# Performance work log

Hardware: AMD Instinct MI355X
Metric: run time of the kernel (lower is better)

Reference implementation:

```python
import jax, jax.numpy as jnp
import numpy as np

MU, SIGMA = -9.1232, 3.5412
FFT_SIZES = [8, 16, 32, 64]
HOP_SIZES = [2, 4, 8, 16]
EPS_MAG, EPS_SC = 1e-7, 1e-8


def hann_periodic(n):
    # torch.hann_window default (periodic=True)
    return 0.5 * (1.0 - jnp.cos(2.0 * jnp.pi * jnp.arange(n, dtype=jnp.float32) / n))


def stft_mag(xf, n_fft, hop):
    # xf: (rows, T). Matches torch.stft(center=True, pad_mode='reflect', onesided).
    pad = n_fft // 2
    xp = jnp.pad(xf, ((0, 0), (pad, pad)), mode='reflect')
    n_frames = 1 + (xp.shape[-1] - n_fft) // hop
    idx = jnp.arange(n_frames)[:, None] * hop + jnp.arange(n_fft)[None, :]
    frames = xp[:, idx] * hann_periodic(n_fft)  # (rows, n_frames, n_fft)
    spec = jnp.fft.rfft(frames, axis=-1)        # (rows, n_frames, n_fft//2+1)
    return jnp.abs(spec) + EPS_MAG


def setup_inputs() -> dict:
    key = jax.random.key(0)
    k1, k2 = jax.random.split(key)
    x = jax.random.normal(k1, (32, 1, 128, 1024), dtype=jnp.float32)
    y = jax.random.normal(k2, (32, 1, 128, 1024), dtype=jnp.float32)
    return {"x": x, "y": y}


def reference(x, y):
    B, C, F_mel, T = x.shape
    x_flat = jnp.exp(x * SIGMA + MU).reshape(-1, T)  # un-normalize log-mel -> linear
    y_flat = jnp.exp(y * SIGMA + MU).reshape(-1, T)
    loss_sc = jnp.float32(0.0)
    loss_mag = jnp.float32(0.0)
    for n_fft, hop in zip(FFT_SIZES, HOP_SIZES):
        x_mag = stft_mag(x_flat, n_fft, hop)
        y_mag = stft_mag(y_flat, n_fft, hop)
        sc = jnp.linalg.norm((y_mag - x_mag).ravel()) / (
            jnp.linalg.norm(y_mag.ravel()) + EPS_SC)
        mag = jnp.mean(jnp.abs(jnp.log(x_mag) - jnp.log(y_mag)))
        loss_sc = loss_sc + sc
        loss_mag = loss_mag + mag
    n = len(FFT_SIZES)
    return (loss_sc / n, loss_mag / n)
```

## Files before the change

kernel.cpp:

```cpp
#include <hip/hip_runtime.h>
#include <math.h>

static constexpr float kSigma = 3.5412f;
static constexpr float kMu    = -9.1232f;

constexpr double kPId = 3.14159265358979323846264338327950288;

constexpr double tp_sin(double r) {
    const double r2 = r * r;
    double t = r, s = r;
    t *= -r2 / (2.0 * 3.0);   s += t;
    t *= -r2 / (4.0 * 5.0);   s += t;
    t *= -r2 / (6.0 * 7.0);   s += t;
    t *= -r2 / (8.0 * 9.0);   s += t;
    t *= -r2 / (10.0 * 11.0); s += t;
    t *= -r2 / (12.0 * 13.0); s += t;
    return s;
}
constexpr double tp_cos(double r) {
    const double r2 = r * r;
    double t = 1.0, c = 1.0;
    t *= -r2 / (1.0 * 2.0);   c += t;
    t *= -r2 / (3.0 * 4.0);   c += t;
    t *= -r2 / (5.0 * 6.0);   c += t;
    t *= -r2 / (7.0 * 8.0);   c += t;
    t *= -r2 / (9.0 * 10.0);  c += t;
    t *= -r2 / (11.0 * 12.0); c += t;
    return c;
}
constexpr float ctw_c(int k, int n) {
    const int kk = ((k % n) + n) % n;
    const int q = (4 * kk) / n;
    const int num = 4 * kk - q * n;
    const double r = (2.0 * kPId * num) / (4.0 * n);
    const double cr = tp_cos(r), sr = tp_sin(r);
    return (float)(q == 0 ? cr : q == 1 ? -sr : q == 2 ? -cr : sr);
}
constexpr float ctw_ns(int k, int n) {
    const int kk = ((k % n) + n) % n;
    const int q = (4 * kk) / n;
    const int num = 4 * kk - q * n;
    const double r = (2.0 * kPId * num) / (4.0 * n);
    const double cr = tp_cos(r), sr = tp_sin(r);
    const double s = (q == 0 ? sr : q == 1 ? cr : q == 2 ? -sr : -cr);
    return (float)(-s);
}

__device__ __forceinline__ float pair_swap(float v) {
    return __int_as_float(__builtin_amdgcn_mov_dpp(__float_as_int(v), 0xB1, 0xF, 0xF, true));
}

#define KA(c) ((c) + ((c) >> 5))

#define DECLZ \
    float zr0=0.f,zi0=0.f, zr1=0.f,zi1=0.f, zr2=0.f,zi2=0.f, zr3=0.f,zi3=0.f, \
          zr4=0.f,zi4=0.f, zr5=0.f,zi5=0.f, zr6=0.f,zi6=0.f, zr7=0.f,zi7=0.f, \
          zr8=0.f,zi8=0.f, zr9=0.f,zi9=0.f, zr10=0.f,zi10=0.f, zr11=0.f,zi11=0.f; \
    (void)zr0;(void)zi0;(void)zr11;(void)zi11;

#define UPDB(n, m) \
    if constexpr ((n) >= 1 && (n) <= NB) { \
        constexpr int   k_ = (BSTART + (n) - 1) * ((m) + TAU * HH); \
        constexpr float c_ = ctw_c(k_, NN); \
        constexpr float s_ = ctw_ns(k_, NN); \
        zr##n = fmaf(d, c_, zr##n);  zi##n = fmaf(d, s_, zi##n); \
    }

#define ALLB(m) UPDB(1,m) UPDB(2,m) UPDB(3,m) UPDB(4,m) UPDB(5,m) \
                UPDB(6,m) UPDB(7,m) UPDB(8,m) UPDB(9,m) UPDB(10,m)

#define UPD_M(m) \
    if constexpr ((m) < HH) { \
        const float d = psb[KA(QB + TAU*HH + NN + (m))] - psb[KA(QB + TAU*HH + (m))]; \
        ALLB(m) \
        if constexpr (((m) & 7) == 7) __builtin_amdgcn_sched_barrier(0); \
    }
#define WRM_M(m) \
    if constexpr ((m) < HH) { \
        const float d = psb[KA(OFF + TAU*HH + (m))]; \
        ALLB(m) \
        if constexpr (((m) & 7) == 7) __builtin_amdgcn_sched_barrier(0); \
    }

#define FORM(M) M(0) M(1) M(2) M(3) M(4) M(5) M(6) M(7) \
                M(8) M(9) M(10) M(11) M(12) M(13) M(14) M(15)

#define EMTB(nm, nc, np) \
    if constexpr (((nc) - 1) >= EJ0 && ((nc) - 1) < EJ0 + EN) { \
        constexpr int BG = BSTART + (nc) - 1; \
        float wr, wi; \
        if constexpr (BG == 0) { \
            const float s_ = (PH==0) ? zr##np : (PH==1) ? -zi##np : (PH==2) ? -zr##np : zi##np; \
            wr = 0.5f*zr##nc - 0.5f*s_;  wi = 0.5f*zi##nc; \
        } else if constexpr (BG == NN/2) { \
            const float s_ = (PH==0) ? zr##nm : (PH==1) ? zi##nm : (PH==2) ? -zr##nm : -zi##nm; \
            wr = 0.5f*zr##nc - 0.5f*s_;  wi = 0.5f*zi##nc; \
        } else { \
            const float tr = (PH==0) ? (zr##nm + zr##np) : (PH==1) ? (zi##nm - zi##np) \
                           : (PH==2) ? (-zr##nm - zr##np) : (zi##np - zi##nm); \
            const float ti = (PH==0) ? (zi##nm + zi##np) : (PH==1) ? (zr##np - zr##nm) \
                           : (PH==2) ? (-zi##nm - zi##np) : (zr##nm - zr##np); \
            wr = fmaf(-0.25f, tr, 0.5f*zr##nc);  wi = fmaf(-0.25f, ti, 0.5f*zi##nc); \
        } \
        const float pm   = fmaf(wr, wr, wi*wi); \
        const float mag  = sqrtf(pm) + 1e-7f; \
        const float lg   = __log2f(mag); \
        const float mago = pair_swap(mag); \
        const float lgo  = pair_swap(lg); \
        const float d_   = mag - mago; \
        sd2 = fmaf(d_, d_, sd2); \
        sy2 = fmaf(mag, mag, sy2); \
        slg += fabsf(lg - lgo); \
    }

#define FOREMT(M) M(0,1,2) M(1,2,3) M(2,3,4) M(3,4,5) M(4,5,6) \
                  M(5,6,7) M(6,7,8) M(7,8,9) M(8,9,10) M(9,10,11)

#define SLOT(q, t) { constexpr int QB = OFF + 4*HH*(q); constexpr int TAU = (t); \
                     constexpr int PH = (t); FOREMT(EMTB) FORM(UPD_M) }
#define SLOT4(q) SLOT(q,0) SLOT(q,1) SLOT(q,2) SLOT(q,3)
#define WARM(t) { constexpr int TAU = (t); FORM(WRM_M) }

template <int NN, int BSTART, int NB, int EJ0, int EN, int OFF, int LOG2SEGS>
__device__ __forceinline__ void run_group(const float* __restrict__ ps0,
                                          int seg, float& sd2, float& sy2, float& slg)
{
    constexpr int HH = NN / 4;
    constexpr int FF = 4096 / NN + 1;
    constexpr int NQ = FF >> (LOG2SEGS + 2);
    static_assert(NQ == 2 || NQ == 4, "unroll pattern assumes NQ in {2,4}");
    const int t0 = (seg * FF) >> LOG2SEGS;
    const int t1 = ((seg + 1) * FF) >> LOG2SEGS;
    const int L  = t1 - t0;
    const int B  = t0 * HH;
    const float* __restrict__ psb = ps0 + B + (B >> 5);

    DECLZ
    WARM(0) WARM(1) WARM(2) WARM(3)

    SLOT4(0) SLOT4(1)
    if constexpr (NQ == 4) { SLOT4(2) SLOT4(3) }
    if (L > 4 * NQ) { SLOT(NQ, 0) }
}

template <int NN, int NGROUPS>
__global__ __launch_bounds__(256, 4)
void sdft_kernel(const float* __restrict__ xg, const float* __restrict__ yg,
                 float* __restrict__ acc )
{
    constexpr int RSTR = (NN == 64) ? 1153 : (NN == 32) ? 1161 : 1160;
    __shared__ float lds[8][RSTR];
    __shared__ float red[4][3];

    const int tid  = threadIdx.x;
    const int row0 = blockIdx.x << 2;

#pragma unroll 1
    for (int task = tid; task < 2048; task += 256) {
        const int q = task & 255, rr = (task >> 8) & 3, sg = task >> 10;
        const float* __restrict__ src = sg ? yg : xg;
        const float4 v = reinterpret_cast<const float4*>(src)[((row0 + rr) << 8) + q];
        const int j = 32 + (q << 2);
        float* dst = &lds[rr * 2 + sg][KA(j)];
        dst[0] = __expf(fmaf(v.x, kSigma, kMu));
        dst[1] = __expf(fmaf(v.y, kSigma, kMu));
        dst[2] = __expf(fmaf(v.z, kSigma, kMu));
        dst[3] = __expf(fmaf(v.w, kSigma, kMu));
    }
#pragma unroll 1
    for (int task = tid; task < 640; task += 256) {
        const int p = task % 80, rem_ = task / 80;
        const int rr = rem_ & 3, sg = rem_ >> 2;
        const int j = (p < 32) ? p : (1024 + p);
        float v = 0.f;
        if (j < 1088) {
            const int i = (j < 32) ? (32 - j) : (2078 - j);
            const float* __restrict__ src = sg ? yg : xg;
            v = __expf(fmaf(src[((row0 + rr) << 10) + i], kSigma, kMu));
        }
        lds[rr * 2 + sg][KA(j)] = v;
    }
    __syncthreads();

    constexpr int GL2 = (NGROUPS == 4) ? 2 : (NGROUPS == 2) ? 1 : 0;
    constexpr int LOG2SEGS = 5 - GL2;
    const int wid  = tid >> 6, lane = tid & 63;
    const int group  = wid & (NGROUPS - 1);
    const int segblk = wid >> GL2;
    const int seg  = (segblk << 3) | (lane >> 3);
    const int sig  = lane & 1;
    const float* ps0 = &lds[lane & 7][0];

    float sd2 = 0.f, sy2 = 0.f, slg = 0.f;
    if constexpr (NN == 64) {
        switch (group) {
            case 0:  run_group<64,  0,  9, 0, 8,  0, LOG2SEGS>(ps0, seg, sd2, sy2, slg); break;
            case 1:  run_group<64,  7, 10, 1, 8,  0, LOG2SEGS>(ps0, seg, sd2, sy2, slg); break;
            case 2:  run_group<64, 15, 10, 1, 8,  0, LOG2SEGS>(ps0, seg, sd2, sy2, slg); break;
            default: run_group<64, 23, 10, 1, 9,  0, LOG2SEGS>(ps0, seg, sd2, sy2, slg); break;
        }
    } else if constexpr (NN == 32) {
        if (group == 0) run_group<32,  0,  9, 0, 8, 16, LOG2SEGS>(ps0, seg, sd2, sy2, slg);
        else            run_group<32,  7, 10, 1, 9, 16, LOG2SEGS>(ps0, seg, sd2, sy2, slg);
    } else if constexpr (NN == 16) {
        run_group<16, 0, 9, 0, 9, 24, LOG2SEGS>(ps0, seg, sd2, sy2, slg);
    } else {
        run_group< 8, 0, 5, 0, 5, 28, LOG2SEGS>(ps0, seg, sd2, sy2, slg);
    }

    if (!sig) sy2 = 0.f;
#pragma unroll
    for (int o = 32; o > 0; o >>= 1) {
        sd2 += __shfl_down(sd2, o);
        sy2 += __shfl_down(sy2, o);
        slg += __shfl_down(slg, o);
    }
    if (lane == 0) { red[wid][0] = sd2; red[wid][1] = sy2; red[wid][2] = slg; }
    __syncthreads();
    if (tid == 0) {
        atomicAdd(&acc[0],   red[0][0] + red[1][0] + red[2][0] + red[3][0]);
        atomicAdd(&acc[64],  red[0][1] + red[1][1] + red[2][1] + red[3][1]);
        atomicAdd(&acc[128], red[0][2] + red[1][2] + red[2][2] + red[3][2]);
    }
}

__global__ void finalize_kernel(const float* __restrict__ acc, float* __restrict__ out)
{
    if (threadIdx.x == 0 && blockIdx.x == 0) {
        const float nel[4] = {10506240.f, 9474048.f, 8982528.f, 8785920.f};
        float sc = 0.f, mg = 0.f;
#pragma unroll
        for (int r = 0; r < 4; ++r) {
            const float a0 = acc[(r * 3 + 0) * 64];
            const float a1 = acc[(r * 3 + 1) * 64];
            const float a2 = acc[(r * 3 + 2) * 64];
            sc += sqrtf(a0 * 0.5f) / (sqrtf(a1) + 1e-8f);
            mg += a2 * 0.34657359028f / nel[r];
        }
        out[0] = sc * 0.25f;
        out[1] = mg * 0.25f;
    }
}

extern "C" void kernel_launch(void* const* d_in, const int* in_sizes, int n_in,
                              void* d_out, int out_size, void* d_ws, size_t ws_size,
                              hipStream_t stream)
{
    const float* x = (const float*)d_in[0];
    const float* y = (const float*)d_in[1];
    float* out = (float*)d_out;
    float* acc = (float*)d_ws;

    hipMemsetAsync(acc, 0, 12 * 64 * sizeof(float), stream);

    sdft_kernel<64, 4><<<1024, 256, 0, stream>>>(x, y, acc + 3 * 192);
    sdft_kernel<32, 2><<<1024, 256, 0, stream>>>(x, y, acc + 2 * 192);
    sdft_kernel<16, 1><<<1024, 256, 0, stream>>>(x, y, acc + 1 * 192);
    sdft_kernel< 8, 1><<<1024, 256, 0, stream>>>(x, y, acc + 0 * 192);

    finalize_kernel<<<1, 64, 0, stream>>>(acc, out);
}
```

Before: 151.7 us.

## Use per-FFT-size LDS padding and per-row phase offsets to avoid bank conflicts

Replaces the fixed 1-in-32 LDS padding with padding of one word every NN entries and adds a per-signal-row offset (phi_seq) so the eight rows read by a wave land in different banks. Because the stride per slot now becomes a loop-carried offp, the fully unrolled SLOT4 macros are collapsed into an unrolled loop. The tail fill loop is generalised to the new padded length. Row strides change, which risks going out of bounds or leaving padding slots uninitialised, and it depends on the bank mapping of mi355x.

```diff
diff --git a/kernel.cpp b/kernel.cpp
--- a/kernel.cpp
+++ b/kernel.cpp
@@ -50,7 +50,11 @@
     return __int_as_float(__builtin_amdgcn_mov_dpp(__float_as_int(v), 0xB1, 0xF, 0xF, true));
 }
 
-#define KA(c) ((c) + ((c) >> 5))
+template <int NN>
+constexpr int phi_seq(int q) {
+    return (NN == 8) ? (((q & 1) << 4) + (q >> 1))
+                     : (((q & 1) << 4) + ((q >> 1) & 1) + ((q & 4) << 1));
+}
 
 #define DECLZ \
     float zr0=0.f,zi0=0.f, zr1=0.f,zi1=0.f, zr2=0.f,zi2=0.f, zr3=0.f,zi3=0.f, \
@@ -69,15 +73,18 @@
 #define ALLB(m) UPDB(1,m) UPDB(2,m) UPDB(3,m) UPDB(4,m) UPDB(5,m) \
                 UPDB(6,m) UPDB(7,m) UPDB(8,m) UPDB(9,m) UPDB(10,m)
 
+#define KAC(c) ((c) + ((c) >> LNN))
+
 #define UPD_M(m) \
     if constexpr ((m) < HH) { \
-        const float d = psb[KA(QB + TAU*HH + NN + (m))] - psb[KA(QB + TAU*HH + (m))]; \
+        const float d = psb[offp + KAC(OFF + TAU*HH + NN + (m))] \
+                      - psb[offp + KAC(OFF + TAU*HH + (m))]; \
         ALLB(m) \
         if constexpr (((m) & 7) == 7) __builtin_amdgcn_sched_barrier(0); \
     }
 #define WRM_M(m) \
     if constexpr ((m) < HH) { \
-        const float d = psb[KA(OFF + TAU*HH + (m))]; \
+        const float d = psb[KAC(OFF + TAU*HH + (m))]; \
         ALLB(m) \
         if constexpr (((m) & 7) == 7) __builtin_amdgcn_sched_barrier(0); \
     }
@@ -116,9 +123,7 @@
 #define FOREMT(M) M(0,1,2) M(1,2,3) M(2,3,4) M(3,4,5) M(4,5,6) \
                   M(5,6,7) M(6,7,8) M(7,8,9) M(8,9,10) M(9,10,11)
 
-#define SLOT(q, t) { constexpr int QB = OFF + 4*HH*(q); constexpr int TAU = (t); \
-                     constexpr int PH = (t); FOREMT(EMTB) FORM(UPD_M) }
-#define SLOT4(q) SLOT(q,0) SLOT(q,1) SLOT(q,2) SLOT(q,3)
+#define SLOT(t) { constexpr int TAU = (t); constexpr int PH = (t); FOREMT(EMTB) FORM(UPD_M) }
 #define WARM(t) { constexpr int TAU = (t); FORM(WRM_M) }
 
 template <int NN, int BSTART, int NB, int EJ0, int EN, int OFF, int LOG2SEGS>
@@ -126,21 +131,25 @@
                                           int seg, float& sd2, float& sy2, float& slg)
 {
     constexpr int HH = NN / 4;
+    constexpr int LNN = (NN == 64) ? 6 : (NN == 32) ? 5 : (NN == 16) ? 4 : 3;
     constexpr int FF = 4096 / NN + 1;
     constexpr int NQ = FF >> (LOG2SEGS + 2);
-    static_assert(NQ == 2 || NQ == 4, "unroll pattern assumes NQ in {2,4}");
     const int t0 = (seg * FF) >> LOG2SEGS;
     const int t1 = ((seg + 1) * FF) >> LOG2SEGS;
     const int L  = t1 - t0;
     const int B  = t0 * HH;
-    const float* __restrict__ psb = ps0 + B + (B >> 5);
+    const float* __restrict__ psb = ps0 + B + (B >> LNN);
 
     DECLZ
     WARM(0) WARM(1) WARM(2) WARM(3)
 
-    SLOT4(0) SLOT4(1)
-    if constexpr (NQ == 4) { SLOT4(2) SLOT4(3) }
-    if (L > 4 * NQ) { SLOT(NQ, 0) }
+    int offp = 0;
+#pragma unroll
+    for (int q = 0; q < NQ; ++q) {
+        SLOT(0) SLOT(1) SLOT(2) SLOT(3)
+        offp += NN + 1;
+    }
+    if (L > 4 * NQ) { SLOT(0) }
 }
 
 template <int NN, int NGROUPS>
@@ -148,7 +157,12 @@
 void sdft_kernel(const float* __restrict__ xg, const float* __restrict__ yg,
                  float* __restrict__ acc )
 {
-    constexpr int RSTR = (NN == 64) ? 1153 : (NN == 32) ? 1161 : 1160;
+    constexpr int LNN  = (NN == 64) ? 6 : (NN == 32) ? 5 : (NN == 16) ? 4 : 3;
+    constexpr int SL   = (NN == 64) ? 1104 : (NN == 32) ? 1080 : (NN == 16) ? 1068 : 1064;
+    constexpr int RSTR = (NN == 64) ? 1152 : (NN == 32) ? 1152 : (NN == 16) ? 1184 : 1216;
+    constexpr int TAIL = SL - 1056;
+    constexpr int PT   = 32 + TAIL;
+
     __shared__ float lds[8][RSTR];
     __shared__ float red[4][3];
 
@@ -161,16 +175,17 @@
         const float* __restrict__ src = sg ? yg : xg;
         const float4 v = reinterpret_cast<const float4*>(src)[((row0 + rr) << 8) + q];
         const int j = 32 + (q << 2);
-        float* dst = &lds[rr * 2 + sg][KA(j)];
+        const int seq = rr * 2 + sg;
+        float* dst = &lds[seq][phi_seq<NN>(seq) + KAC(j)];
         dst[0] = __expf(fmaf(v.x, kSigma, kMu));
         dst[1] = __expf(fmaf(v.y, kSigma, kMu));
         dst[2] = __expf(fmaf(v.z, kSigma, kMu));
         dst[3] = __expf(fmaf(v.w, kSigma, kMu));
     }
 #pragma unroll 1
-    for (int task = tid; task < 640; task += 256) {
-        const int p = task % 80, rem_ = task / 80;
-        const int rr = rem_ & 3, sg = rem_ >> 2;
+    for (int task = tid; task < 8 * PT; task += 256) {
+        const int p = task % PT, seq = task / PT;
+        const int rr = seq >> 1, sg = seq & 1;
         const int j = (p < 32) ? p : (1024 + p);
         float v = 0.f;
         if (j < 1088) {
@@ -178,7 +193,7 @@
             const float* __restrict__ src = sg ? yg : xg;
             v = __expf(fmaf(src[((row0 + rr) << 10) + i], kSigma, kMu));
         }
-        lds[rr * 2 + sg][KA(j)] = v;
+        lds[seq][phi_seq<NN>(seq) + KAC(j)] = v;
     }
     __syncthreads();
 
@@ -189,7 +204,8 @@
     const int segblk = wid >> GL2;
     const int seg  = (segblk << 3) | (lane >> 3);
     const int sig  = lane & 1;
-    const float* ps0 = &lds[lane & 7][0];
+    const int seq  = lane & 7;
+    const float* ps0 = &lds[seq][phi_seq<NN>(seq)];
 
     float sd2 = 0.f, sy2 = 0.f, slg = 0.f;
     if constexpr (NN == 64) {
```

After: 143.7 us. 1.06x faster.
